# Optimization experiments

Measured on AMD Instinct MI355X. Metric: run time of the kernel, lower is better.

Reference implementation:

```python
import jax, jax.numpy as jnp
import numpy as np

NBITS = 8
REDUCE = 64
OUT = 512


def setup_inputs() -> dict:
    key = jax.random.key(0)
    ks = jax.random.split(key, 6)
    T, B, C = 512, 16, 512
    ne = 2 ** NBITS
    x = jax.random.normal(ks[0], (T, B, C), dtype=jnp.float32)
    key_in = jax.random.normal(ks[1], (T, B, C), dtype=jnp.float32)  # unused by forward (overwritten)
    # xavier-ish init scales
    map_w = jax.random.normal(ks[2], (NBITS, C), dtype=jnp.float32) * np.sqrt(2.0 / (C + NBITS))
    map_b = jnp.zeros((NBITS,), dtype=jnp.float32)
    pw_w1 = jax.random.normal(ks[3], (REDUCE, C), dtype=jnp.float32) * np.sqrt(2.0 / (C + REDUCE))
    pw_w21 = jax.random.normal(ks[4], (ne, OUT * REDUCE), dtype=jnp.float32) * np.sqrt(2.0 / (ne + OUT * REDUCE))
    pw_w22 = jax.random.normal(ks[5], (ne, OUT * REDUCE), dtype=jnp.float32) * np.sqrt(2.0 / (ne + OUT * REDUCE))
    pw_B = jnp.zeros((1, 1, OUT), dtype=jnp.float32)
    return {"x": x, "key": key_in, "map_w": map_w, "map_b": map_b,
            "pw_w1": pw_w1, "pw_w21": pw_w21, "pw_w22": pw_w22, "pw_B": pw_B}


def reference(x, key, map_w, map_b, pw_w1, pw_w21, pw_w22, pw_B):
    # x: (T,B,C). `key` arg is overwritten by x in the original source.
    T, B, C = x.shape
    nbits = map_w.shape[0]
    out_dim = pw_B.shape[-1]
    reduce_dim = pw_w1.shape[0]

    k = x.reshape(T * B, C) @ map_w.T + map_b          # (T*B, nbits)
    z = jnp.clip(1.2 * jax.nn.sigmoid(k) - 0.1, 0.0, 1.0)  # saturated sigmoid
    code = (z > 0.5).astype(z.dtype)                   # eval: hard binary code

    pows = (2 ** jnp.arange(nbits, dtype=jnp.int32))   # bit_to_int weights
    qz1 = jnp.sum(code.astype(jnp.int32) * pows, axis=-1)          # (T*B,)
    qz2 = jnp.sum((1 - code.astype(jnp.int32)) * pows, axis=-1)    # (T*B,)

    # gather per-token expert rows and synthesize per-token weight matrix
    w2 = (pw_w21[qz1] + pw_w22[qz2]).reshape(T, B, out_dim, reduce_dim)

    # original computes (w2 @ pw_w1) @ x; reassociated as w2 @ (pw_w1 @ x)
    # to avoid materializing the (T,B,out,in) intermediate (same math)
    v = jnp.einsum('ri,tbi->tbr', pw_w1, x)            # (T,B,reduce)
    y = jnp.einsum('tbor,tbr->tbo', w2, v) + pw_B      # (T,B,out)

    loss = jnp.zeros((1,), dtype=x.dtype)
    return (y, loss)
```

## Files before the change

### kernel.cpp

```cpp
#include <hip/hip_runtime.h>

#define NTOK 8192
#define CDIM 512
#define NB   8
#define RD   64
#define OD   512

typedef unsigned char  u8;
typedef unsigned int   u32;
typedef unsigned short u16;

#define WS_Q      0
#define WS_COUNTS 8192
#define WS_CURSOR 9216
#define WS_OFF    10240
#define WS_LIST   11520
#define WS_V      28672
#define WS_NEED   (WS_V + NTOK * RD * 4)

__global__ __launch_bounds__(256) void kInit(u32* __restrict__ counts) {
    counts[threadIdx.x] = 0u;
}

__global__ __launch_bounds__(256) void kA(
    const float* __restrict__ x, const float* __restrict__ map_w,
    const float* __restrict__ map_b, const float* __restrict__ w1,
    u8* __restrict__ q_out, float* __restrict__ v_out,
    u32* __restrict__ counts, float* __restrict__ loss_out)
{
    const int t    = threadIdx.x;
    const int lane = t & 63;
    const int wv   = __builtin_amdgcn_readfirstlane(t >> 6);
    const int b    = blockIdx.x;

    if (b < 512) {
        const int tg  = b >> 2;
        const int rg  = b & 3;
        const int tok = tg * 64 + lane;
        const int r0  = __builtin_amdgcn_readfirstlane(rg * 16 + wv * 4);
        const float4* __restrict__ x4 = (const float4*)x + (size_t)tok * (CDIM / 4);
        const float4* __restrict__ w4 = (const float4*)w1;
        float a0 = 0.f, a1 = 0.f, a2 = 0.f, a3 = 0.f;
        #pragma unroll 4
        for (int k = 0; k < CDIM / 4; ++k) {
            float4 xv = x4[k];
            float4 w0 = w4[(size_t)(r0 + 0) * (CDIM / 4) + k];
            float4 w1v = w4[(size_t)(r0 + 1) * (CDIM / 4) + k];
            float4 w2 = w4[(size_t)(r0 + 2) * (CDIM / 4) + k];
            float4 w3 = w4[(size_t)(r0 + 3) * (CDIM / 4) + k];
            a0 += w0.x * xv.x + w0.y * xv.y + w0.z * xv.z + w0.w * xv.w;
            a1 += w1v.x * xv.x + w1v.y * xv.y + w1v.z * xv.z + w1v.w * xv.w;
            a2 += w2.x * xv.x + w2.y * xv.y + w2.z * xv.z + w2.w * xv.w;
            a3 += w3.x * xv.x + w3.y * xv.y + w3.z * xv.z + w3.w * xv.w;
        }
        float4 o = make_float4(a0, a1, a2, a3);
        *((float4*)(v_out + (size_t)tok * RD + r0)) = o;
    } else {
        const int tg  = b - 512;
        const int tok = tg * 64 + lane;
        __shared__ u32 qs[64];
        if (t < 64) qs[t] = 0u;
        __syncthreads();

        const int b0 = __builtin_amdgcn_readfirstlane(2 * wv);
        const int b1 = b0 + 1;
        const float4* __restrict__ x4 = (const float4*)x + (size_t)tok * (CDIM / 4);
        const float4* __restrict__ m4 = (const float4*)map_w;
        double s0 = 0.0, s1 = 0.0;
        for (int k = 0; k < CDIM / 4; ++k) {
            float4 xv = x4[k];
            float4 m0 = m4[(size_t)b0 * (CDIM / 4) + k];
            float4 m1 = m4[(size_t)b1 * (CDIM / 4) + k];
            s0 += (double)m0.x * (double)xv.x + (double)m0.y * (double)xv.y
                + (double)m0.z * (double)xv.z + (double)m0.w * (double)xv.w;
            s1 += (double)m1.x * (double)xv.x + (double)m1.y * (double)xv.y
                + (double)m1.z * (double)xv.z + (double)m1.w * (double)xv.w;
        }
        s0 += (double)map_b[b0];
        s1 += (double)map_b[b1];
        unsigned long long m0 = __ballot(s0 > 0.0);
        unsigned long long m1 = __ballot(s1 > 0.0);
        u32 bits = (u32)(((m0 >> lane) & 1ull) | (((m1 >> lane) & 1ull) << 1)) << (2 * wv);
        if (bits) atomicOr(&qs[lane], bits);
        __syncthreads();
        if (t < 64) {
            u32 q = qs[t];
            q_out[tok] = (u8)q;
            atomicAdd(&counts[q], 1u);
        }
        if (b == 512 && t == 0) loss_out[0] = 0.0f;
    }
}

__global__ __launch_bounds__(256) void kPrefix(
    const u32* __restrict__ counts, u32* __restrict__ off, u32* __restrict__ cursor)
{
    __shared__ u32 s[256];
    const int t = threadIdx.x;
    u32 c = counts[t];
    s[t] = c;
    __syncthreads();
    for (int d = 1; d < 256; d <<= 1) {
        u32 v = (t >= d) ? s[t - d] : 0u;
        __syncthreads();
        s[t] += v;
        __syncthreads();
    }
    u32 excl = s[t] - c;
    off[t] = excl;
    cursor[t] = excl;
    if (t == 255) off[256] = s[255];
}

__global__ __launch_bounds__(256) void kScatter(
    const u8* __restrict__ q_arr, u32* __restrict__ cursor, u16* __restrict__ list)
{
    const int tok = blockIdx.x * 256 + threadIdx.x;
    u32 pos = atomicAdd(&cursor[q_arr[tok]], 1u);
    list[pos] = (u16)tok;
}

__global__ __launch_bounds__(256) void kB(
    const u16* __restrict__ list, const u32* __restrict__ off,
    const float* __restrict__ v_arr,
    const float* __restrict__ w21, const float* __restrict__ w22,
    const float* __restrict__ pwB, float* __restrict__ y)
{
    const int q  = blockIdx.x >> 1;
    const int oh = blockIdx.x & 1;
    const int o  = oh * 256 + threadIdx.x;
    const u32 lo = off[q], hi = off[q + 1];
    if (lo == hi) return;

    const float4* __restrict__ pa = (const float4*)(w21 + ((size_t)q * OD + o) * RD);
    const float4* __restrict__ pb = (const float4*)(w22 + ((size_t)(255 - q) * OD + o) * RD);
    float w[RD];
    #pragma unroll
    for (int j = 0; j < RD / 4; ++j) {
        float4 a = pa[j], bb = pb[j];
        w[j * 4 + 0] = a.x + bb.x;
        w[j * 4 + 1] = a.y + bb.y;
        w[j * 4 + 2] = a.z + bb.z;
        w[j * 4 + 3] = a.w + bb.w;
    }
    const float bias = pwB[o];

    for (u32 i = lo; i < hi; ++i) {
        const int tok = __builtin_amdgcn_readfirstlane((int)list[i]);
        const float4* __restrict__ vr = (const float4*)(v_arr + (size_t)tok * RD);
        float acc = bias;
        #pragma unroll
        for (int j = 0; j < RD / 4; ++j) {
            float4 vv = vr[j];
            acc += w[j * 4 + 0] * vv.x + w[j * 4 + 1] * vv.y
                 + w[j * 4 + 2] * vv.z + w[j * 4 + 3] * vv.w;
        }
        y[(size_t)tok * OD + o] = acc;
    }
}

__global__ __launch_bounds__(256) void mono(
    const float* __restrict__ x, const float* __restrict__ map_w,
    const float* __restrict__ map_b, const float* __restrict__ w1,
    const float* __restrict__ w21, const float* __restrict__ w22,
    const float* __restrict__ pwB, float* __restrict__ y)
{
    const int tok = blockIdx.x;
    const int t   = threadIdx.x;
    __shared__ float xsh[CDIM];
    __shared__ float vsh[RD];
    __shared__ int qsh;

    if (t == 0) qsh = 0;
    for (int i = t; i < CDIM; i += 256) xsh[i] = x[(size_t)tok * CDIM + i];
    __syncthreads();

    if (t < NB) {
        double a = 0.0;
        const float* mrow = map_w + (size_t)t * CDIM;
        for (int j = 0; j < CDIM; ++j) a += (double)mrow[j] * (double)xsh[j];
        a += (double)map_b[t];
        if (a > 0.0) atomicOr(&qsh, 1 << t);
    }
    if (t < RD) {
        const float* wrow = w1 + (size_t)t * CDIM;
        float acc = 0.f;
        for (int j = 0; j < CDIM; ++j) acc += wrow[j] * xsh[j];
        vsh[t] = acc;
    }
    __syncthreads();

    const int q = qsh;
    for (int o = t; o < OD; o += 256) {
        const float* pa = w21 + (size_t)q * (OD * RD) + (size_t)o * RD;
        const float* pb = w22 + (size_t)(255 - q) * (OD * RD) + (size_t)o * RD;
        float acc = pwB[o];
        for (int r = 0; r < RD; ++r) acc += (pa[r] + pb[r]) * vsh[r];
        y[(size_t)tok * OD + o] = acc;
    }
    if (tok == 0 && t == 0) y[(size_t)NTOK * OD] = 0.0f;
}

extern "C" void kernel_launch(void* const* d_in, const int* in_sizes, int n_in,
                              void* d_out, int out_size, void* d_ws, size_t ws_size,
                              hipStream_t stream) {
    const float* x     = (const float*)d_in[0];
    const float* map_w = (const float*)d_in[2];
    const float* map_b = (const float*)d_in[3];
    const float* w1    = (const float*)d_in[4];
    const float* w21   = (const float*)d_in[5];
    const float* w22   = (const float*)d_in[6];
    const float* pwB   = (const float*)d_in[7];
    float* out = (float*)d_out;

    if (ws_size >= (size_t)WS_NEED) {
        char* ws = (char*)d_ws;
        u8*    q_ws   = (u8*)(ws + WS_Q);
        u32*   counts = (u32*)(ws + WS_COUNTS);
        u32*   cursor = (u32*)(ws + WS_CURSOR);
        u32*   off    = (u32*)(ws + WS_OFF);
        u16*   list   = (u16*)(ws + WS_LIST);
        float* v_ws   = (float*)(ws + WS_V);

        kInit<<<1, 256, 0, stream>>>(counts);
        kA<<<640, 256, 0, stream>>>(x, map_w, map_b, w1, q_ws, v_ws, counts,
                                    out + (size_t)NTOK * OD);
        kPrefix<<<1, 256, 0, stream>>>(counts, off, cursor);
        kScatter<<<NTOK / 256, 256, 0, stream>>>(q_ws, cursor, list);
        kB<<<512, 256, 0, stream>>>(list, off, v_ws, w21, w22, pwB, out);
    } else {
        mono<<<NTOK, 256, 0, stream>>>(x, map_w, map_b, w1, w21, w22, pwB, out);
    }
}
```

Before: 222.0 us.

## Restructure projection kernel per token tile and split expert GEMV across token halves

kA now processes 16 tokens per block: x rows are staged in shared memory, two waves compute the 64-dim reduce projection for 8 tokens each with lane-per-output-row, and two waves compute the 8 hash bits from shared x. kB splits each expert bucket's token list across two blocks, caches token ids in LDS, and processes four tokens per iteration to raise memory-level parallelism. This aims to cut redundant global x/w1 reads and improve occupancy on the skewed per-expert work, at the cost of more LDS use and uncoalesced w1 row reads per lane.

```diff
diff --git a/kernel.cpp b/kernel.cpp
--- a/kernel.cpp
+++ b/kernel.cpp
@@ -5,6 +5,7 @@
 #define NB   8
 #define RD   64
 #define OD   512
+#define XROW 516
 
 typedef unsigned char  u8;
 typedef unsigned int   u32;
@@ -29,67 +30,68 @@
     u32* __restrict__ counts, float* __restrict__ loss_out)
 {
     const int t    = threadIdx.x;
+    const int tok0 = blockIdx.x * 16;
+    __shared__ float xs[16 * XROW];
+
+    const float4* __restrict__ xsrc = (const float4*)(x + (size_t)tok0 * CDIM);
+    #pragma unroll
+    for (int u = 0; u < 8; ++u) {
+        int i = u * 256 + t;
+        int r = i >> 7, c = i & 127;
+        *(float4*)(xs + r * XROW + c * 4) = xsrc[i];
+    }
+    __syncthreads();
+
+    const int wvu  = __builtin_amdgcn_readfirstlane(t >> 6);
     const int lane = t & 63;
-    const int wv   = __builtin_amdgcn_readfirstlane(t >> 6);
-    const int b    = blockIdx.x;
-
-    if (b < 512) {
-        const int tg  = b >> 2;
-        const int rg  = b & 3;
-        const int tok = tg * 64 + lane;
-        const int r0  = __builtin_amdgcn_readfirstlane(rg * 16 + wv * 4);
-        const float4* __restrict__ x4 = (const float4*)x + (size_t)tok * (CDIM / 4);
-        const float4* __restrict__ w4 = (const float4*)w1;
-        float a0 = 0.f, a1 = 0.f, a2 = 0.f, a3 = 0.f;
-        #pragma unroll 4
-        for (int k = 0; k < CDIM / 4; ++k) {
-            float4 xv = x4[k];
-            float4 w0 = w4[(size_t)(r0 + 0) * (CDIM / 4) + k];
-            float4 w1v = w4[(size_t)(r0 + 1) * (CDIM / 4) + k];
-            float4 w2 = w4[(size_t)(r0 + 2) * (CDIM / 4) + k];
-            float4 w3 = w4[(size_t)(r0 + 3) * (CDIM / 4) + k];
-            a0 += w0.x * xv.x + w0.y * xv.y + w0.z * xv.z + w0.w * xv.w;
-            a1 += w1v.x * xv.x + w1v.y * xv.y + w1v.z * xv.z + w1v.w * xv.w;
-            a2 += w2.x * xv.x + w2.y * xv.y + w2.z * xv.z + w2.w * xv.w;
-            a3 += w3.x * xv.x + w3.y * xv.y + w3.z * xv.z + w3.w * xv.w;
-        }
-        float4 o = make_float4(a0, a1, a2, a3);
-        *((float4*)(v_out + (size_t)tok * RD + r0)) = o;
+
+    if (wvu < 2) {
+        const int tb = tok0 + wvu * 8;
+        const float4* __restrict__ w4  = (const float4*)w1 + (size_t)lane * 128;
+        const float4* __restrict__ xg  = (const float4*)x + (size_t)tb * 128;
+        float a0=0.f,a1=0.f,a2=0.f,a3=0.f,a4=0.f,a5=0.f,a6=0.f,a7=0.f;
+        for (int k = 0; k < 128; ++k) {
+            float4 w = w4[k];
+            float4 x0 = xg[0*128+k], x1 = xg[1*128+k], x2 = xg[2*128+k], x3 = xg[3*128+k];
+            float4 x4v = xg[4*128+k], x5 = xg[5*128+k], x6 = xg[6*128+k], x7 = xg[7*128+k];
+            a0 += w.x*x0.x + w.y*x0.y + w.z*x0.z + w.w*x0.w;
+            a1 += w.x*x1.x + w.y*x1.y + w.z*x1.z + w.w*x1.w;
+            a2 += w.x*x2.x + w.y*x2.y + w.z*x2.z + w.w*x2.w;
+            a3 += w.x*x3.x + w.y*x3.y + w.z*x3.z + w.w*x3.w;
+            a4 += w.x*x4v.x + w.y*x4v.y + w.z*x4v.z + w.w*x4v.w;
+            a5 += w.x*x5.x + w.y*x5.y + w.z*x5.z + w.w*x5.w;
+            a6 += w.x*x6.x + w.y*x6.y + w.z*x6.z + w.w*x6.w;
+            a7 += w.x*x7.x + w.y*x7.y + w.z*x7.z + w.w*x7.w;
+        }
+        v_out[(size_t)(tb+0) * RD + lane] = a0;
+        v_out[(size_t)(tb+1) * RD + lane] = a1;
+        v_out[(size_t)(tb+2) * RD + lane] = a2;
+        v_out[(size_t)(tb+3) * RD + lane] = a3;
+        v_out[(size_t)(tb+4) * RD + lane] = a4;
+        v_out[(size_t)(tb+5) * RD + lane] = a5;
+        v_out[(size_t)(tb+6) * RD + lane] = a6;
+        v_out[(size_t)(tb+7) * RD + lane] = a7;
     } else {
-        const int tg  = b - 512;
-        const int tok = tg * 64 + lane;
-        __shared__ u32 qs[64];
-        if (t < 64) qs[t] = 0u;
-        __syncthreads();
-
-        const int b0 = __builtin_amdgcn_readfirstlane(2 * wv);
-        const int b1 = b0 + 1;
-        const float4* __restrict__ x4 = (const float4*)x + (size_t)tok * (CDIM / 4);
-        const float4* __restrict__ m4 = (const float4*)map_w;
-        double s0 = 0.0, s1 = 0.0;
-        for (int k = 0; k < CDIM / 4; ++k) {
-            float4 xv = x4[k];
-            float4 m0 = m4[(size_t)b0 * (CDIM / 4) + k];
-            float4 m1 = m4[(size_t)b1 * (CDIM / 4) + k];
-            s0 += (double)m0.x * (double)xv.x + (double)m0.y * (double)xv.y
-                + (double)m0.z * (double)xv.z + (double)m0.w * (double)xv.w;
-            s1 += (double)m1.x * (double)xv.x + (double)m1.y * (double)xv.y
-                + (double)m1.z * (double)xv.z + (double)m1.w * (double)xv.w;
-        }
-        s0 += (double)map_b[b0];
-        s1 += (double)map_b[b1];
-        unsigned long long m0 = __ballot(s0 > 0.0);
-        unsigned long long m1 = __ballot(s1 > 0.0);
-        u32 bits = (u32)(((m0 >> lane) & 1ull) | (((m1 >> lane) & 1ull) << 1)) << (2 * wv);
-        if (bits) atomicOr(&qs[lane], bits);
-        __syncthreads();
-        if (t < 64) {
-            u32 q = qs[t];
-            q_out[tok] = (u8)q;
-            atomicAdd(&counts[q], 1u);
-        }
-        if (b == 512 && t == 0) loss_out[0] = 0.0f;
-    }
+        const int lt  = t - 128;
+        const int tk  = lt >> 3;
+        const int bit = lt & 7;
+        const float4* __restrict__ m4 = (const float4*)map_w + (size_t)bit * 128;
+        const float4* __restrict__ xl = (const float4*)(xs + tk * XROW);
+        double s = 0.0;
+        for (int k = 0; k < 128; ++k) {
+            float4 m = m4[k], xv = xl[k];
+            s += (double)m.x * (double)xv.x + (double)m.y * (double)xv.y
+               + (double)m.z * (double)xv.z + (double)m.w * (double)xv.w;
+        }
+        s += (double)map_b[bit];
+        unsigned long long mask = __ballot(s > 0.0);
+        if (bit == 0) {
+            u32 qv = (u32)((mask >> ((tk & 7) * 8)) & 0xFFull);
+            q_out[tok0 + tk] = (u8)qv;
+            atomicAdd(&counts[qv], 1u);
+        }
+    }
+    if (blockIdx.x == 0 && t == 0) loss_out[0] = 0.0f;
 }
 
 __global__ __launch_bounds__(256) void kPrefix(
@@ -126,36 +128,61 @@
     const float* __restrict__ w21, const float* __restrict__ w22,
     const float* __restrict__ pwB, float* __restrict__ y)
 {
-    const int q  = blockIdx.x >> 1;
-    const int oh = blockIdx.x & 1;
-    const int o  = oh * 256 + threadIdx.x;
+    const int q  = blockIdx.x >> 2;
+    const int oh = (blockIdx.x >> 1) & 1;
+    const int th = blockIdx.x & 1;
+    const int t  = threadIdx.x;
+    const int o  = oh * 256 + t;
+
     const u32 lo = off[q], hi = off[q + 1];
-    if (lo == hi) return;
+    const int n = (int)(hi - lo);
+    if (n == 0) return;
+    const int half = (n + 1) >> 1;
+    const int s0   = th * half;
+    const int cnt  = min(n - s0, half);
+    if (cnt <= 0) return;
+
+    __shared__ u16 ltok[4096];
+    for (int i = t; i < cnt; i += 256) ltok[i] = list[lo + s0 + i];
 
     const float4* __restrict__ pa = (const float4*)(w21 + ((size_t)q * OD + o) * RD);
     const float4* __restrict__ pb = (const float4*)(w22 + ((size_t)(255 - q) * OD + o) * RD);
-    float w[RD];
+    float4 w[16];
     #pragma unroll
-    for (int j = 0; j < RD / 4; ++j) {
-        float4 a = pa[j], bb = pb[j];
-        w[j * 4 + 0] = a.x + bb.x;
-        w[j * 4 + 1] = a.y + bb.y;
-        w[j * 4 + 2] = a.z + bb.z;
-        w[j * 4 + 3] = a.w + bb.w;
+    for (int j = 0; j < 16; ++j) {
+        float4 a = pa[j], b = pb[j];
+        w[j] = make_float4(a.x + b.x, a.y + b.y, a.z + b.z, a.w + b.w);
     }
     const float bias = pwB[o];
-
-    for (u32 i = lo; i < hi; ++i) {
-        const int tok = __builtin_amdgcn_readfirstlane((int)list[i]);
-        const float4* __restrict__ vr = (const float4*)(v_arr + (size_t)tok * RD);
-        float acc = bias;
+    __syncthreads();
+
+    const float4* __restrict__ v4 = (const float4*)v_arr;
+    for (int i = 0; i < cnt; i += 4) {
+        const int nb = cnt - i;
+        const int i1 = (nb > 1) ? i + 1 : i;
+        const int i2 = (nb > 2) ? i + 2 : i;
+        const int i3 = (nb > 3) ? i + 3 : i;
+        const int t0 = __builtin_amdgcn_readfirstlane((int)ltok[i]);
+        const int t1 = __builtin_amdgcn_readfirstlane((int)ltok[i1]);
+        const int t2 = __builtin_amdgcn_readfirstlane((int)ltok[i2]);
+        const int t3 = __builtin_amdgcn_readfirstlane((int)ltok[i3]);
+        const float4* __restrict__ p0 = v4 + (size_t)t0 * 16;
+        const float4* __restrict__ p1 = v4 + (size_t)t1 * 16;
+        const float4* __restrict__ p2 = v4 + (size_t)t2 * 16;
+        const float4* __restrict__ p3 = v4 + (size_t)t3 * 16;
+        float a0 = bias, a1 = bias, a2 = bias, a3 = bias;
         #pragma unroll
-        for (int j = 0; j < RD / 4; ++j) {
-            float4 vv = vr[j];
-            acc += w[j * 4 + 0] * vv.x + w[j * 4 + 1] * vv.y
-                 + w[j * 4 + 2] * vv.z + w[j * 4 + 3] * vv.w;
-        }
-        y[(size_t)tok * OD + o] = acc;
+        for (int j = 0; j < 16; ++j) {
+            float4 ww = w[j];
+            float4 v0 = p0[j]; a0 += ww.x*v0.x + ww.y*v0.y + ww.z*v0.z + ww.w*v0.w;
+            float4 v1 = p1[j]; a1 += ww.x*v1.x + ww.y*v1.y + ww.z*v1.z + ww.w*v1.w;
+            float4 v2 = p2[j]; a2 += ww.x*v2.x + ww.y*v2.y + ww.z*v2.z + ww.w*v2.w;
+            float4 v3 = p3[j]; a3 += ww.x*v3.x + ww.y*v3.y + ww.z*v3.z + ww.w*v3.w;
+        }
+        y[(size_t)t0 * OD + o] = a0;
+        if (nb > 1) y[(size_t)t1 * OD + o] = a1;
+        if (nb > 2) y[(size_t)t2 * OD + o] = a2;
+        if (nb > 3) y[(size_t)t3 * OD + o] = a3;
     }
 }
 
@@ -223,11 +250,11 @@
         float* v_ws   = (float*)(ws + WS_V);
 
         kInit<<<1, 256, 0, stream>>>(counts);
-        kA<<<640, 256, 0, stream>>>(x, map_w, map_b, w1, q_ws, v_ws, counts,
-                                    out + (size_t)NTOK * OD);
+        kA<<<NTOK / 16, 256, 0, stream>>>(x, map_w, map_b, w1, q_ws, v_ws, counts,
+                                          out + (size_t)NTOK * OD);
         kPrefix<<<1, 256, 0, stream>>>(counts, off, cursor);
         kScatter<<<NTOK / 256, 256, 0, stream>>>(q_ws, cursor, list);
-        kB<<<512, 256, 0, stream>>>(list, off, v_ws, w21, w22, pwB, out);
+        kB<<<1024, 256, 0, stream>>>(list, off, v_ws, w21, w22, pwB, out);
     } else {
         mono<<<NTOK, 256, 0, stream>>>(x, map_w, map_b, w1, w21, w22, pwB, out);
     }
```

New measurement: 223.4 us. Within noise of the previous version (+0.7%).
